# Optimization experiments

Measured on AMD Instinct MI355X. Metric: run time of the kernel, lower is better.

Reference implementation:

```python
import math
import jax, jax.numpy as jnp
import numpy as np

NUM_HEADS = 12


def _key_blocks(x, w):
    # x: [B,S,H,D] -> overlapping key blocks [B, C, 3w, H, D], block c covers
    # original key positions [c*w - w, c*w + 2w) (zero padded at the edges).
    B, S, H, D = x.shape
    C = S // w
    x_pad = jnp.pad(x, ((0, 0), (w, w), (0, 0), (0, 0)))
    idx = (jnp.arange(C) * w)[:, None] + jnp.arange(3 * w)[None, :]  # [C,3w]
    return x_pad[:, idx]


def _band_qk(q, k, w):
    # banded_gemm_qk: scores[b,i,h,j] = q[b,i,h,:] . k[b,i+j-w,h,:], j in [0,2w]
    B, S, H, D = q.shape
    C = S // w
    kb = _key_blocks(k, w)                       # [B,C,3w,H,D]
    qb = q.reshape(B, C, w, H, D)
    s = jnp.einsum('bcxhd,bcyhd->bchxy', qb, kb)  # [B,C,H,w,3w]
    row = jnp.arange(w)[:, None]
    col = row + jnp.arange(2 * w + 1)[None, :]    # diagonal extraction
    band = s[:, :, :, row, col]                   # [B,C,H,w,2w+1]
    return band.transpose(0, 1, 3, 2, 4).reshape(B, S, H, 2 * w + 1)


def _band_pv(p, v, w):
    # banded_gemm_pv: out[b,i,h,:] = sum_j p[b,i,h,j] * v[b,i+j-w,h,:]
    B, S, H, M = p.shape
    C = S // w
    vb = _key_blocks(v, w)                        # [B,C,3w,H,D]
    pb = p.reshape(B, C, w, H, M).transpose(0, 1, 3, 2, 4)  # [B,C,H,w,2w+1]
    row = jnp.arange(w)[:, None]
    col = row + jnp.arange(2 * w + 1)[None, :]
    p_full = jnp.zeros((B, C, H, w, 3 * w), p.dtype).at[:, :, :, row, col].set(pb)
    out = jnp.einsum('bchxy,bcyhd->bcxhd', p_full, vb)  # [B,C,w,H,D]
    return out.reshape(B, S, H, -1)


def setup_inputs():
    key = jax.random.key(0)
    ks = jax.random.split(key, 14)
    B, S, E, G = 2, 4096, 768, 64
    scale = 0.02
    hs = jax.random.normal(ks[0], (B, S, E), jnp.float32)
    mask = jnp.zeros((B, 1, 1, S), jnp.int32).at[:, :, :, :G].set(1)
    def lin(k):
        kw, kb = jax.random.split(k)
        return (jax.random.normal(kw, (E, E), jnp.float32) * scale,
                jax.random.normal(kb, (E,), jnp.float32) * scale)
    Wq, bq = lin(ks[1]); Wk, bk = lin(ks[2]); Wv, bv = lin(ks[3])
    Wqg, bqg = lin(ks[4]); Wkg, bkg = lin(ks[5]); Wvg, bvg = lin(ks[6])
    return dict(hidden_states=hs, attention_mask=mask,
                Wq=Wq, bq=bq, Wk=Wk, bk=bk, Wv=Wv, bv=bv,
                Wqg=Wqg, bqg=bqg, Wkg=Wkg, bkg=bkg, Wvg=Wvg, bvg=bvg,
                window=256, num_global=G)


def reference(hidden_states, attention_mask, Wq, bq, Wk, bk, Wv, bv,
              Wqg, bqg, Wkg, bkg, Wvg, bvg, window, num_global):
    B, S, E = hidden_states.shape
    H = NUM_HEADS
    D = E // H
    w, G = window, num_global
    inv_sqrt_d = 1.0 / math.sqrt(D)

    mask2d = attention_mask.reshape(B, S)
    removed = mask2d != 0  # global (or padding) keys excluded from windowed attn

    q = (hidden_states @ Wq + bq) * inv_sqrt_d
    k = hidden_states @ Wk + bk
    v = hidden_states @ Wv + bv
    q = q.reshape(B, S, H, D)
    k = k.reshape(B, S, H, D)
    v = v.reshape(B, S, H, D)

    # --- local (banded) attention scores ---
    band = _band_qk(q, k, w)                                  # [B,S,H,2w+1]
    key_pos = jnp.arange(S)[:, None] + jnp.arange(-w, w + 1)[None, :]  # [S,2w+1]
    valid = (key_pos >= 0) & (key_pos < S)
    removed_pad = jnp.pad(removed, ((0, 0), (w, w)))
    band_removed = removed_pad[:, key_pos + w]                # [B,S,2w+1]
    keep = valid[None, :, None, :] & (~band_removed)[:, :, None, :]
    band = jnp.where(keep, band, -jnp.inf)

    # --- every-token -> global-token scores (global tokens are first G) ---
    sel = jnp.einsum('blhd,bshd->blhs', q, k[:, :G])          # [B,S,H,G]
    scores = jnp.concatenate([sel, band], axis=-1)            # [B,S,H,G+2w+1]
    probs = jax.nn.softmax(scores.astype(jnp.float32), axis=-1)

    out = jnp.einsum('blhs,bshd->blhd', probs[..., :G], v[:, :G].astype(jnp.float32))
    out = out + _band_pv(probs[..., G:], v.astype(jnp.float32), w)
    out = out.astype(hidden_states.dtype).reshape(B, S, E)

    # --- global tokens attend to everything (separate projections) ---
    hg = hidden_states[:, :G]
    qg = (hg @ Wqg + bqg).reshape(B, G, H, D)
    kg = (hidden_states @ Wkg + bkg).reshape(B, S, H, D)
    vg = (hidden_states @ Wvg + bvg).reshape(B, S, H, D)
    gs = jnp.einsum('bghd,bshd->bhgs', qg, kg) * inv_sqrt_d   # [B,H,G,S]
    gp = jax.nn.softmax(gs.astype(jnp.float32), axis=-1)
    go = jnp.einsum('bhgs,bshd->bghd', gp, vg.astype(jnp.float32)).reshape(B, G, E)
    out = out.at[:, :G].set(go.astype(out.dtype))
    return out
```

## Files before the change

kernel.cpp:

```cpp
#include <hip/hip_runtime.h>
#include <hip/hip_bf16.h>


#define BB 2
#define SS 4096
#define EE 768
#define HH 12
#define DD 64
#define WW 256
#define GG 64
#define NSPLIT 16

typedef unsigned short u16;
typedef __attribute__((ext_vector_type(4))) float f4v;
typedef __attribute__((ext_vector_type(8))) short s8v;
typedef __attribute__((ext_vector_type(4))) int i4v;
typedef __attribute__((ext_vector_type(4))) unsigned short us4v;

#define MFMA_BF16(a, b, c) __builtin_amdgcn_mfma_f32_16x16x32_bf16((a), (b), (c), 0, 0, 0)

constexpr long NSE     = (long)BB * SS * EE;
constexpr long OFF_HSB = 0;
constexpr long OFF_WT  = OFF_HSB + NSE;
constexpr long OFF_Q   = OFF_WT + 6L * EE * EE;
constexpr long OFF_K   = OFF_Q + NSE;
constexpr long OFF_V   = OFF_K + NSE;
constexpr long OFF_KG  = OFF_V + NSE;
constexpr long OFF_VG  = OFF_KG + NSE;
constexpr long OFF_QG  = OFF_VG + NSE;
constexpr long OFF_VT  = OFF_QG + (long)BB * GG * EE;
constexpr long OFF_VGT = OFF_VT + NSE;

constexpr long NQTILE = (long)BB * HH * 4;

__device__ __forceinline__ u16 f2bf(float f) {
  unsigned u = __float_as_uint(f);
  u += 0x7fffu + ((u >> 16) & 1u);
  return (u16)(u >> 16);
}

__device__ __forceinline__ void gload_lds16(const u16* g, u16* l) {
  __builtin_amdgcn_global_load_lds(
      (const __attribute__((address_space(1))) void*)g,
      (__attribute__((address_space(3))) void*)l, 16, 0, 0);
}

__global__ __launch_bounds__(256) void k_prep(const float* __restrict__ hs,
                                              const float* __restrict__ Wq, const float* __restrict__ Wk,
                                              const float* __restrict__ Wv, const float* __restrict__ Wkg,
                                              const float* __restrict__ Wvg, const float* __restrict__ Wqg,
                                              u16* __restrict__ ws) {
  int bid = blockIdx.x;
  if (bid < 6144) {
    long i = ((long)bid * 256 + threadIdx.x) * 4;
    f4v v = *(const f4v*)(hs + i);
    us4v o;
#pragma unroll
    for (int j = 0; j < 4; ++j) o[j] = f2bf(v[j]);
    *(us4v*)(ws + OFF_HSB + i) = o;
    return;
  }
  int wb = bid - 6144;
  int widx = wb / 576; int rem = wb % 576; int kt = rem / 24; int nt = rem % 24;
  const float* src;
  switch (widx) {
    case 0: src = Wq; break; case 1: src = Wk; break; case 2: src = Wv; break;
    case 3: src = Wkg; break; case 4: src = Wvg; break; default: src = Wqg; break;
  }
  __shared__ float tl[32][33];
  int t = threadIdx.x; int r = t >> 3; int c4 = (t & 7) * 4;
  f4v v = *(const f4v*)(src + (long)(kt * 32 + r) * EE + nt * 32 + c4);
#pragma unroll
  for (int j = 0; j < 4; ++j) tl[r][c4 + j] = v[j];
  __syncthreads();
  us4v o;
#pragma unroll
  for (int j = 0; j < 4; ++j) o[j] = f2bf(tl[c4 + j][r]);
  *(us4v*)(ws + OFF_WT + (long)widx * EE * EE + (long)(nt * 32 + r) * EE + kt * 32 + c4) = o;
}

__global__ __launch_bounds__(256, 4) void k_proj(u16* __restrict__ ws,
                                              const float* __restrict__ bq, const float* __restrict__ bk,
                                              const float* __restrict__ bv, const float* __restrict__ bkg,
                                              const float* __restrict__ bvg, const float* __restrict__ bqg) {
  int bid = blockIdx.x;
  int widx, mt, nt;
  if (bid < 1920) {
    int L = (bid & 7) * 240 + (bid >> 3);
    mt = L / 30; int inner = L % 30; widx = inner / 6; nt = inner % 6;
  } else { widx = 5; mt = 0; nt = bid - 1920; }

  __shared__ u16 Al[128 * 64];
  __shared__ u16 Bl[128 * 64];
  int tid = threadIdx.x, lane = tid & 63, wid = tid >> 6;
  int wr = wid >> 1, wc = wid & 1;

  f4v acc[4][4];
#pragma unroll
  for (int i = 0; i < 4; ++i)
#pragma unroll
    for (int j = 0; j < 4; ++j) acc[i][j] = f4v{0.f, 0.f, 0.f, 0.f};

  const u16* hsb = ws + OFF_HSB;
  const u16* Wp  = ws + OFF_WT + (long)widx * EE * EE;

  const u16* asrc[4]; const u16* bsrc[4];
  u16* adst[4]; u16* bdst[4];
#pragma unroll
  for (int it = 0; it < 4; ++it) {
    int c = tid + it * 256;
    int r = c >> 3, o8 = (c & 7) * 8;
    long arow;
    if (widx == 5) { int rr = mt * 128 + r; arow = (long)(rr >> 6) * SS + (rr & 63); }
    else           { arow = (long)mt * 128 + r; }
    asrc[it] = hsb + arow * EE + o8;
    bsrc[it] = Wp + (long)(nt * 128 + r) * EE + o8;
    adst[it] = Al + c * 8;
    bdst[it] = Bl + c * 8;
  }

  const u16* afp[4]; const u16* bfp[4];
#pragma unroll
  for (int f = 0; f < 4; ++f) {
    afp[f] = Al + (wr * 64 + f * 16 + (lane & 15)) * 64 + (lane >> 4) * 8;
    bfp[f] = Bl + (wc * 64 + f * 16 + (lane & 15)) * 64 + (lane >> 4) * 8;
  }

  for (int k0 = 0; k0 < EE; k0 += 64) {
#pragma unroll
    for (int it = 0; it < 4; ++it) {
      gload_lds16(asrc[it] + k0, adst[it]);
      gload_lds16(bsrc[it] + k0, bdst[it]);
    }
    __syncthreads();
#pragma unroll
    for (int ks = 0; ks < 2; ++ks) {
      s8v af[4], bfr[4];
#pragma unroll
      for (int f = 0; f < 4; ++f) {
        af[f]  = *(const s8v*)(afp[f] + ks * 32);
        bfr[f] = *(const s8v*)(bfp[f] + ks * 32);
      }
#pragma unroll
      for (int i = 0; i < 4; ++i)
#pragma unroll
        for (int j = 0; j < 4; ++j) acc[i][j] = MFMA_BF16(af[i], bfr[j], acc[i][j]);
    }
    __syncthreads();
  }

  const float* bias; u16* outp; float scl = 1.0f;
  switch (widx) {
    case 0: bias = bq;  outp = ws + OFF_Q;  scl = 0.125f * 1.44269504f; break;
    case 1: bias = bk;  outp = ws + OFF_K;  break;
    case 2: bias = bv;  outp = ws + OFF_VT;  break;
    case 3: bias = bkg; outp = ws + OFF_KG; break;
    case 4: bias = bvg; outp = ws + OFF_VGT; break;
    default: bias = bqg; outp = ws + OFF_QG; scl = 0.125f; break;
  }

  if (widx == 2 || widx == 4) {
    int s0g = mt * 128 + wr * 64 + (lane >> 4) * 4;
#pragma unroll
    for (int fi = 0; fi < 4; ++fi) {
      int srow = s0g + fi * 16;
      int b_ = srow >> 12; int sl = srow & (SS - 1);
#pragma unroll
      for (int fj = 0; fj < 4; ++fj) {
        int col = nt * 128 + wc * 64 + fj * 16 + (lane & 15);
        float bcol = bias[col];
        us4v o;
#pragma unroll
        for (int e = 0; e < 4; ++e) o[e] = f2bf(acc[fi][fj][e] + bcol);
        *(us4v*)&outp[((long)(b_ * HH + (col >> 6)) * DD + (col & 63)) * SS + sl] = o;
      }
    }
  } else {
#pragma unroll
    for (int fi = 0; fi < 4; ++fi)
#pragma unroll
      for (int fj = 0; fj < 4; ++fj) {
        int col = nt * 128 + wc * 64 + fj * 16 + (lane & 15);
        float bcol = bias[col];
#pragma unroll
        for (int e = 0; e < 4; ++e) {
          int rl = wr * 64 + fi * 16 + (lane >> 4) * 4 + e;
          float vv = (acc[fi][fj][e] + bcol) * scl;
          outp[(long)(mt * 128 + rl) * EE + col] = f2bf(vv);
        }
      }
  }
}

__global__ __launch_bounds__(256) void k_lattn(const u16* __restrict__ ws, float* __restrict__ out) {
  int bid0 = blockIdx.x;
  int bid = (bid0 & 7) * 189 + (bid0 >> 3);
  int b = bid / (HH * 63); int rem = bid % (HH * 63); int h = rem / 63; int qt = rem % 63;
  int l0 = GG + qt * 64;
  int tid = threadIdx.x, lane = tid & 63, wid = tid >> 6;

  __shared__ u16 Kl[64][72];
  __shared__ u16 Vtl[64][72];
  __shared__ u16 Pl[4][16][72];

  const u16* Qp  = ws + OFF_Q + (long)b * SS * EE;
  const u16* Kp  = ws + OFF_K + (long)b * SS * EE;
  const u16* Vtp = ws + OFF_VT + (long)(b * HH + h) * DD * SS;

  int qbase = l0 + wid * 16;
  s8v qf[2];
#pragma unroll
  for (int ks = 0; ks < 2; ++ks)
    qf[ks] = *(const s8v*)(Qp + (long)(qbase + (lane & 15)) * EE + h * DD + ks * 32 + (lane >> 4) * 8);

  float m_r[4], l_p[4]; f4v ao[4];
#pragma unroll
  for (int e = 0; e < 4; ++e) { m_r[e] = -1e30f; l_p[e] = 0.f; }
#pragma unroll
  for (int df = 0; df < 4; ++df) ao[df] = f4v{0.f, 0.f, 0.f, 0.f};

  int lo = (l0 - WW > GG) ? (l0 - WW) : GG;
  int hi = (l0 + 64 + WW < SS) ? (l0 + 64 + WW) : SS;
  int ntile = 1 + ((hi - lo) >> 6);

  const u16* kbase[2]; const u16* vbase[2];
  u16* kdst[2]; u16* vdst[2];
#pragma unroll
  for (int it = 0; it < 2; ++it) {
    int c = tid + it * 256;
    int sr = c >> 3, so = (c & 7) * 8;
    kbase[it] = Kp + (long)sr * EE + h * DD + so;
    vbase[it] = Vtp + (long)sr * SS + so;
    kdst[it] = &Kl[sr][so];
    vdst[it] = &Vtl[sr][so];
  }

  i4v kreg[2], vreg[2];
#pragma unroll
  for (int it = 0; it < 2; ++it) {
    kreg[it] = *(const i4v*)(kbase[it]);
    vreg[it] = *(const i4v*)(vbase[it]);
  }
#pragma unroll
  for (int it = 0; it < 2; ++it) {
    *(i4v*)kdst[it] = kreg[it];
    *(i4v*)vdst[it] = vreg[it];
  }
  __syncthreads();

  for (int t = 0; t < ntile; ++t) {
    int kb = (t == 0) ? 0 : lo + (t - 1) * 64;
    if (t + 1 < ntile) {
      int kbn = lo + t * 64;
#pragma unroll
      for (int it = 0; it < 2; ++it) {
        kreg[it] = *(const i4v*)(kbase[it] + (long)kbn * EE);
        vreg[it] = *(const i4v*)(vbase[it] + kbn);
      }
    }

    f4v sc[4];
#pragma unroll
    for (int c = 0; c < 4; ++c) sc[c] = f4v{0.f, 0.f, 0.f, 0.f};
    __builtin_amdgcn_s_setprio(1);
#pragma unroll
    for (int c = 0; c < 4; ++c)
#pragma unroll
      for (int ks = 0; ks < 2; ++ks) {
        s8v kf = *(const s8v*)&Kl[c * 16 + (lane & 15)][ks * 32 + (lane >> 4) * 8];
        sc[c] = MFMA_BF16(qf[ks], kf, sc[c]);
      }
    __builtin_amdgcn_s_setprio(0);

    if (t > 0 && (kb <= l0 - WW || kb >= l0 + WW)) {
#pragma unroll
      for (int c = 0; c < 4; ++c) {
        int key = kb + c * 16 + (lane & 15);
#pragma unroll
        for (int e = 0; e < 4; ++e) {
          int qrow = qbase + (lane >> 4) * 4 + e;
          if (key < qrow - WW || key > qrow + WW) sc[c][e] = -1e30f;
        }
      }
    }

    float pmax[4];
#pragma unroll
    for (int e = 0; e < 4; ++e)
      pmax[e] = fmaxf(fmaxf(sc[0][e], sc[1][e]), fmaxf(sc[2][e], sc[3][e]));
    bool need;
    if (t == 0) need = true;
    else {
      bool ok = (pmax[0] <= m_r[0] + 11.5f) & (pmax[1] <= m_r[1] + 11.5f) &
                (pmax[2] <= m_r[2] + 11.5f) & (pmax[3] <= m_r[3] + 11.5f);
      need = !__all(ok);
    }
    if (need) {
#pragma unroll
      for (int e = 0; e < 4; ++e) {
        float rm = pmax[e];
#pragma unroll
        for (int off = 1; off < 16; off <<= 1) rm = fmaxf(rm, __shfl_xor(rm, off));
        float mn = fmaxf(m_r[e], rm);
        float scl = exp2f(m_r[e] - mn);
        l_p[e] *= scl;
#pragma unroll
        for (int df = 0; df < 4; ++df) ao[df][e] *= scl;
        m_r[e] = mn;
      }
    }

#pragma unroll
    for (int e = 0; e < 4; ++e) {
      float p0 = exp2f(sc[0][e] - m_r[e]);
      float p1 = exp2f(sc[1][e] - m_r[e]);
      float p2 = exp2f(sc[2][e] - m_r[e]);
      float p3 = exp2f(sc[3][e] - m_r[e]);
      l_p[e] += (p0 + p1) + (p2 + p3);
      int pr = (lane >> 4) * 4 + e;
      Pl[wid][pr][(lane & 15)]      = f2bf(p0);
      Pl[wid][pr][16 + (lane & 15)] = f2bf(p1);
      Pl[wid][pr][32 + (lane & 15)] = f2bf(p2);
      Pl[wid][pr][48 + (lane & 15)] = f2bf(p3);
    }

    __builtin_amdgcn_s_setprio(1);
#pragma unroll
    for (int kblk = 0; kblk < 2; ++kblk) {
      s8v pf = *(const s8v*)&Pl[wid][lane & 15][kblk * 32 + (lane >> 4) * 8];
#pragma unroll
      for (int df = 0; df < 4; ++df) {
        s8v vf = *(const s8v*)&Vtl[df * 16 + (lane & 15)][kblk * 32 + (lane >> 4) * 8];
        ao[df] = MFMA_BF16(pf, vf, ao[df]);
      }
    }
    __builtin_amdgcn_s_setprio(0);
    __syncthreads();

    if (t + 1 < ntile) {
#pragma unroll
      for (int it = 0; it < 2; ++it) {
        *(i4v*)kdst[it] = kreg[it];
        *(i4v*)vdst[it] = vreg[it];
      }
    }
    __syncthreads();
  }

  float l_r[4];
#pragma unroll
  for (int e = 0; e < 4; ++e) {
    float s = l_p[e];
#pragma unroll
    for (int off = 1; off < 16; off <<= 1) s += __shfl_xor(s, off);
    l_r[e] = s;
  }
#pragma unroll
  for (int df = 0; df < 4; ++df)
#pragma unroll
    for (int e = 0; e < 4; ++e) {
      int row = qbase + (lane >> 4) * 4 + e;
      int col = h * DD + df * 16 + (lane & 15);
      out[((long)b * SS + row) * EE + col] = ao[df][e] / l_r[e];
    }
}

__global__ __launch_bounds__(64) void k_gattn_part(u16* __restrict__ ws) {
  int bid = blockIdx.x;
  int g = bid / NSPLIT; int sp = bid % NSPLIT;
  int b = g / (HH * 4); int rem = g % (HH * 4); int h = rem >> 2; int qs = rem & 3;
  int lane = threadIdx.x;

  __shared__ u16 Kl[32][72];
  __shared__ u16 Vtl[64][40];
  __shared__ u16 Pl[16][40];

  const u16* Qgp = ws + OFF_QG + (long)b * GG * EE;
  const u16* Kgp = ws + OFF_KG + (long)b * SS * EE;
  const u16* Vtp = ws + OFF_VGT + (long)(b * HH + h) * DD * SS;

  int qbase = qs * 16;
  s8v qf[2];
#pragma unroll
  for (int ks = 0; ks < 2; ++ks)
    qf[ks] = *(const s8v*)(Qgp + (long)(qbase + (lane & 15)) * EE + h * DD + ks * 32 + (lane >> 4) * 8);

  float m_r[4], l_r[4]; f4v ao[4];
#pragma unroll
  for (int e = 0; e < 4; ++e) { m_r[e] = -1e30f; l_r[e] = 0.f; }
#pragma unroll
  for (int df = 0; df < 4; ++df) ao[df] = f4v{0.f, 0.f, 0.f, 0.f};

  int t0 = sp * (SS / 32 / NSPLIT);
  for (int kt = t0; kt < t0 + SS / 32 / NSPLIT; ++kt) {
    int kb = kt * 32;
#pragma unroll
    for (int r2 = 0; r2 < 4; ++r2) {
      int chunk = lane + r2 * 64;
      int kr = chunk >> 3, ko = (chunk & 7) * 8;
      *(i4v*)&Kl[kr][ko] = *(const i4v*)(Kgp + (long)(kb + kr) * EE + h * DD + ko);
      int dr = chunk >> 2, ko2 = (chunk & 3) * 8;
      *(i4v*)&Vtl[dr][ko2] = *(const i4v*)(Vtp + (long)dr * SS + kb + ko2);
    }
    __syncthreads();

    f4v sc[2] = {f4v{0.f, 0.f, 0.f, 0.f}, f4v{0.f, 0.f, 0.f, 0.f}};
#pragma unroll
    for (int c = 0; c < 2; ++c)
#pragma unroll
      for (int ks = 0; ks < 2; ++ks) {
        s8v kf = *(const s8v*)&Kl[c * 16 + (lane & 15)][ks * 32 + (lane >> 4) * 8];
        sc[c] = MFMA_BF16(qf[ks], kf, sc[c]);
      }

    float scl_[4], p0[4], p1[4];
#pragma unroll
    for (int e = 0; e < 4; ++e) {
      float rm = fmaxf(sc[0][e], sc[1][e]);
#pragma unroll
      for (int off = 1; off < 16; off <<= 1) rm = fmaxf(rm, __shfl_xor(rm, off));
      float mn = fmaxf(m_r[e], rm);
      scl_[e] = __expf(m_r[e] - mn);
      p0[e] = __expf(sc[0][e] - mn);
      p1[e] = __expf(sc[1][e] - mn);
      float s = p0[e] + p1[e];
#pragma unroll
      for (int off = 1; off < 16; off <<= 1) s += __shfl_xor(s, off);
      l_r[e] = l_r[e] * scl_[e] + s;
      m_r[e] = mn;
    }
#pragma unroll
    for (int df = 0; df < 4; ++df)
#pragma unroll
      for (int e = 0; e < 4; ++e) ao[df][e] *= scl_[e];

#pragma unroll
    for (int e = 0; e < 4; ++e) {
      Pl[(lane >> 4) * 4 + e][lane & 15]        = f2bf(p0[e]);
      Pl[(lane >> 4) * 4 + e][16 + (lane & 15)] = f2bf(p1[e]);
    }
    s8v pf = *(const s8v*)&Pl[lane & 15][(lane >> 4) * 8];
#pragma unroll
    for (int df = 0; df < 4; ++df) {
      s8v vf = *(const s8v*)&Vtl[df * 16 + (lane & 15)][(lane >> 4) * 8];
      ao[df] = MFMA_BF16(pf, vf, ao[df]);
    }
    __syncthreads();
  }

  float* PA = (float*)(ws + OFF_V);
  float* Pm = PA + NQTILE * NSPLIT * 1024L;
  float* Pl2 = Pm + NQTILE * NSPLIT * 16L;
  long pb = (long)g * NSPLIT + sp;
#pragma unroll
  for (int df = 0; df < 4; ++df)
#pragma unroll
    for (int e = 0; e < 4; ++e) {
      int rl = (lane >> 4) * 4 + e;
      PA[pb * 1024 + rl * 64 + df * 16 + (lane & 15)] = ao[df][e];
    }
  if ((lane & 15) == 0) {
#pragma unroll
    for (int e = 0; e < 4; ++e) {
      int rl = (lane >> 4) * 4 + e;
      Pm[pb * 16 + rl] = m_r[e];
      Pl2[pb * 16 + rl] = l_r[e];
    }
  }
}

__global__ __launch_bounds__(256) void k_gattn_comb(const u16* __restrict__ ws, float* __restrict__ out) {
  int g = blockIdx.x;
  int b = g / (HH * 4); int rem = g % (HH * 4); int h = rem >> 2; int qs = rem & 3;
  int tid = threadIdx.x;
  int row = tid >> 4; int c4 = (tid & 15) * 4;

  const float* PA = (const float*)(ws + OFF_V);
  const float* Pm = PA + NQTILE * NSPLIT * 1024L;
  const float* Pl2 = Pm + NQTILE * NSPLIT * 16L;
  long base = (long)g * NSPLIT;

  float M = -1e30f;
#pragma unroll
  for (int s = 0; s < NSPLIT; ++s) M = fmaxf(M, Pm[(base + s) * 16 + row]);
  f4v acc = f4v{0.f, 0.f, 0.f, 0.f};
  float L = 0.f;
#pragma unroll
  for (int s = 0; s < NSPLIT; ++s) {
    float wgt = __expf(Pm[(base + s) * 16 + row] - M);
    L += wgt * Pl2[(base + s) * 16 + row];
    f4v a = *(const f4v*)&PA[(base + s) * 1024 + row * 64 + c4];
#pragma unroll
    for (int j = 0; j < 4; ++j) acc[j] += wgt * a[j];
  }
  float inv = 1.f / L;
  f4v o;
#pragma unroll
  for (int j = 0; j < 4; ++j) o[j] = acc[j] * inv;
  *(f4v*)&out[((long)b * SS + qs * 16 + row) * EE + h * DD + c4] = o;
}

extern "C" void kernel_launch(void* const* d_in, const int* in_sizes, int n_in,
                              void* d_out, int out_size, void* d_ws, size_t ws_size,
                              hipStream_t stream) {
  const float* hs  = (const float*)d_in[0];
  const float* Wq  = (const float*)d_in[2];  const float* bq  = (const float*)d_in[3];
  const float* Wk  = (const float*)d_in[4];  const float* bk  = (const float*)d_in[5];
  const float* Wv  = (const float*)d_in[6];  const float* bv  = (const float*)d_in[7];
  const float* Wqg = (const float*)d_in[8];  const float* bqg = (const float*)d_in[9];
  const float* Wkg = (const float*)d_in[10]; const float* bkg = (const float*)d_in[11];
  const float* Wvg = (const float*)d_in[12]; const float* bvg = (const float*)d_in[13];
  u16* ws = (u16*)d_ws;
  float* out = (float*)d_out;

  k_prep<<<6144 + 6 * 24 * 24, 256, 0, stream>>>(hs, Wq, Wk, Wv, Wkg, Wvg, Wqg, ws);
  k_proj<<<1926, 256, 0, stream>>>(ws, bq, bk, bv, bkg, bvg, bqg);
  k_gattn_part<<<(int)(NQTILE * NSPLIT), 64, 0, stream>>>(ws);
  k_gattn_comb<<<(int)NQTILE, 256, 0, stream>>>(ws, out);
  k_lattn<<<BB * HH * 63, 256, 0, stream>>>(ws, out);
}
```

Measured before the change: 155.8 us.

## Prefetch projection GEMM tiles into registers and XOR-swizzle LDS layout

The projection GEMM stops using direct global-to-LDS loads followed by a barrier. It now loads the next K tile into registers while the MFMAs run on the current LDS tile, then writes that tile to LDS. The LDS layout is XOR-swizzled by row so the 16-byte fragment reads avoid bank conflicts. This costs extra VGPRs for the staging registers and adds an explicit LDS store step per iteration.

Measured after the change: 154.8 us. No clear change (-0.6%).

```diff
diff --git a/kernel.cpp b/kernel.cpp
--- a/kernel.cpp
+++ b/kernel.cpp
@@ -39,12 +39,6 @@
   return (u16)(u >> 16);
 }
 
-__device__ __forceinline__ void gload_lds16(const u16* g, u16* l) {
-  __builtin_amdgcn_global_load_lds(
-      (const __attribute__((address_space(1))) void*)g,
-      (__attribute__((address_space(3))) void*)l, 16, 0, 0);
-}
-
 __global__ __launch_bounds__(256) void k_prep(const float* __restrict__ hs,
                                               const float* __restrict__ Wq, const float* __restrict__ Wk,
                                               const float* __restrict__ Wv, const float* __restrict__ Wkg,
@@ -105,46 +99,70 @@
   const u16* Wp  = ws + OFF_WT + (long)widx * EE * EE;
 
   const u16* asrc[4]; const u16* bsrc[4];
-  u16* adst[4]; u16* bdst[4];
+  int dso[4];
 #pragma unroll
   for (int it = 0; it < 4; ++it) {
     int c = tid + it * 256;
-    int r = c >> 3, o8 = (c & 7) * 8;
+    int r = c >> 3, j = c & 7;
     long arow;
     if (widx == 5) { int rr = mt * 128 + r; arow = (long)(rr >> 6) * SS + (rr & 63); }
     else           { arow = (long)mt * 128 + r; }
-    asrc[it] = hsb + arow * EE + o8;
-    bsrc[it] = Wp + (long)(nt * 128 + r) * EE + o8;
-    adst[it] = Al + c * 8;
-    bdst[it] = Bl + c * 8;
+    asrc[it] = hsb + arow * EE + j * 8;
+    bsrc[it] = Wp + (long)(nt * 128 + r) * EE + j * 8;
+    dso[it]  = r * 64 + (j ^ (r & 7)) * 8;
   }
 
   const u16* afp[4]; const u16* bfp[4];
 #pragma unroll
   for (int f = 0; f < 4; ++f) {
-    afp[f] = Al + (wr * 64 + f * 16 + (lane & 15)) * 64 + (lane >> 4) * 8;
-    bfp[f] = Bl + (wc * 64 + f * 16 + (lane & 15)) * 64 + (lane >> 4) * 8;
-  }
-
-  for (int k0 = 0; k0 < EE; k0 += 64) {
-#pragma unroll
-    for (int it = 0; it < 4; ++it) {
-      gload_lds16(asrc[it] + k0, adst[it]);
-      gload_lds16(bsrc[it] + k0, bdst[it]);
+    afp[f] = Al + (wr * 64 + f * 16 + (lane & 15)) * 64;
+    bfp[f] = Bl + (wc * 64 + f * 16 + (lane & 15)) * 64;
+  }
+  int hi4 = lane >> 4, lx = lane & 7;
+
+  i4v areg[4], breg[4];
+#pragma unroll
+  for (int it = 0; it < 4; ++it) {
+    areg[it] = *(const i4v*)(asrc[it]);
+    breg[it] = *(const i4v*)(bsrc[it]);
+  }
+#pragma unroll
+  for (int it = 0; it < 4; ++it) {
+    *(i4v*)&Al[dso[it]] = areg[it];
+    *(i4v*)&Bl[dso[it]] = breg[it];
+  }
+  __syncthreads();
+
+  for (int t = 0; t < 12; ++t) {
+    if (t < 11) {
+      int k0n = (t + 1) * 64;
+#pragma unroll
+      for (int it = 0; it < 4; ++it) {
+        areg[it] = *(const i4v*)(asrc[it] + k0n);
+        breg[it] = *(const i4v*)(bsrc[it] + k0n);
+      }
+    }
+#pragma unroll
+    for (int ks = 0; ks < 2; ++ks) {
+      int sw = ((ks * 4 + hi4) ^ lx) * 8;
+      s8v af[4], bfr[4];
+#pragma unroll
+      for (int f = 0; f < 4; ++f) {
+        af[f]  = *(const s8v*)(afp[f] + sw);
+        bfr[f] = *(const s8v*)(bfp[f] + sw);
+      }
+#pragma unroll
+      for (int i = 0; i < 4; ++i)
+#pragma unroll
+        for (int j = 0; j < 4; ++j) acc[i][j] = MFMA_BF16(af[i], bfr[j], acc[i][j]);
     }
     __syncthreads();
-#pragma unroll
-    for (int ks = 0; ks < 2; ++ks) {
-      s8v af[4], bfr[4];
-#pragma unroll
-      for (int f = 0; f < 4; ++f) {
-        af[f]  = *(const s8v*)(afp[f] + ks * 32);
-        bfr[f] = *(const s8v*)(bfp[f] + ks * 32);
-      }
-#pragma unroll
-      for (int i = 0; i < 4; ++i)
-#pragma unroll
-        for (int j = 0; j < 4; ++j) acc[i][j] = MFMA_BF16(af[i], bfr[j], acc[i][j]);
+    if (t < 11) {
+#pragma unroll
+      for (int it = 0; it < 4; ++it) {
+        *(i4v*)&Al[dso[it]] = areg[it];
+        *(i4v*)&Bl[dso[it]] = breg[it];
+      }
     }
     __syncthreads();
   }
```
